# Kernel tuning notes

Hardware: AMD Instinct MI355X
Metric: run time of the kernel (lower is better)

Reference implementation:

```python
import jax, jax.numpy as jnp
import numpy as np

N = 100000   # nodes
E = 1600000  # edges
F_IN = 128
H = 128
C = 40


def setup_inputs() -> dict:
    key = jax.random.key(0)
    ks = jax.random.split(key, 8)
    s = 0.05
    return {
        "x": jax.random.normal(ks[0], (N, F_IN), dtype=jnp.float32),
        "edge_index": jax.random.randint(ks[1], (2, E), 0, N, dtype=jnp.int32),
        "W1": jax.random.normal(ks[2], (F_IN, H), dtype=jnp.float32) * s,
        "b1": jnp.zeros((H,), jnp.float32),
        "W2": jax.random.normal(ks[3], (H, H), dtype=jnp.float32) * s,
        "b2": jnp.zeros((H,), jnp.float32),
        "Wfc": jax.random.normal(ks[4], (H, C), dtype=jnp.float32) * s,
        "bfc": jnp.zeros((C,), jnp.float32),
    }


def _graph_conv(x, src, dst, norm_out, norm_in, W, b):
    # DGL GraphConv, norm='both': h = D_in^{-1/2} A D_out^{-1/2} x W + b
    h = (x * norm_out[:, None]) @ W                      # [N, H] (W first: in>=out)
    agg = jax.ops.segment_sum(h[src], dst, num_segments=N)  # gather + scatter-add
    return agg * norm_in[:, None] + b


def reference(x, edge_index, W1, b1, W2, b2, Wfc, bfc):
    src, dst = edge_index[0], edge_index[1]
    ones = jnp.ones((E,), x.dtype)
    deg_out = jnp.maximum(jax.ops.segment_sum(ones, src, num_segments=N), 1.0)
    deg_in = jnp.maximum(jax.ops.segment_sum(ones, dst, num_segments=N), 1.0)
    norm_out = jax.lax.rsqrt(deg_out)
    norm_in = jax.lax.rsqrt(deg_in)
    # layer 0: GraphConv + relu (dropout is identity in eval mode)
    h = jax.nn.relu(_graph_conv(x, src, dst, norm_out, norm_in, W1, b1))
    # layer 1: GraphConv, no activation
    h = _graph_conv(h, src, dst, norm_out, norm_in, W2, b2)
    # final FC
    return h @ Wfc + bfc
```

## Files before the change

### kernel.cpp

```cpp
#include <hip/hip_runtime.h>
#include <hip/hip_fp16.h>


#define CHUNK    8192
#define NBK      800
#define SLAB     3072

typedef __attribute__((ext_vector_type(8))) short bf16x8;
typedef __attribute__((ext_vector_type(4))) float f32x4;

struct __align__(8)  half4 { __half x, y, z, w; };
struct __align__(16) half8 { __half h[8]; };

__device__ __forceinline__ unsigned short f2bf(float f) {
    union { float f; unsigned u; } v; v.f = f;
    unsigned r = v.u + 0x7FFFu + ((v.u >> 16) & 1u);
    return (unsigned short)(r >> 16);
}
__device__ __forceinline__ float bf2f(unsigned short h) {
    union { unsigned u; float f; } v; v.u = ((unsigned)h) << 16;
    return v.f;
}

__global__ void setup_kernel(const float* __restrict__ W1, const float* __restrict__ W2,
                             const float* __restrict__ Wfc,
                             const float* __restrict__ b2, const float* __restrict__ bfc,
                             unsigned short* __restrict__ Wh1, unsigned short* __restrict__ Wl1,
                             unsigned short* __restrict__ Wh2, unsigned short* __restrict__ Wl2,
                             float* __restrict__ b2p,
                             int* __restrict__ cur_d, int* __restrict__ deg_out,
                             int nbuck, int N_) {
    int idx = blockIdx.x * blockDim.x + threadIdx.x;
    if (idx < nbuck) cur_d[idx] = idx * SLAB;
    for (int i = idx; i < N_; i += gridDim.x * blockDim.x) deg_out[i] = 0;

    if (idx < 16384) {
        int k = idx >> 7, nn = idx & 127;
        float v = W1[idx];
        int q = k >> 5, j = k & 7, lb = ((k >> 3) & 3) * 16;
        int tcol = nn >> 4;
        int l = lb + (nn & 15);
        int pos = ((tcol * 4 + q) * 64 + l) * 8 + j;
        unsigned short h = f2bf(v);
        Wh1[pos] = h;
        Wl1[pos] = f2bf(v - bf2f(h));
    } else if (idx < 16384 + 6144) {
        int i2 = idx - 16384;
        int k = i2 / 48, nn = i2 - k * 48;
        float v = 0.f;
        if (nn < 40) {
            const float* w2row = W2 + k * 128;
            #pragma unroll 8
            for (int jj = 0; jj < 128; ++jj) v += w2row[jj] * Wfc[jj * 40 + nn];
        }
        int t = nn >> 4, q = k >> 5, j = k & 7;
        int l = ((k >> 3) & 3) * 16 + (nn & 15);
        int pos = ((t * 4 + q) * 64 + l) * 8 + j;
        unsigned short h = f2bf(v);
        Wh2[pos] = h;
        Wl2[pos] = f2bf(v - bf2f(h));
    } else if (idx < 16384 + 6144 + 40) {
        int c = idx - (16384 + 6144);
        float a = bfc[c];
        #pragma unroll 8
        for (int j = 0; j < 128; ++j) a += b2[j] * Wfc[j * 40 + c];
        b2p[c] = a;
    }
}

__global__ __launch_bounds__(256) void scatter_res_kernel(
        const int* __restrict__ src, const int* __restrict__ dst,
        int* __restrict__ cur_d, int* __restrict__ deg_out,
        unsigned int* __restrict__ ppack, int E) {
    __shared__ int hd[NBK], bd[NBK];
    const int tid = threadIdx.x;
    for (int i = tid; i < NBK; i += 256) hd[i] = 0;
    __syncthreads();
    const int base = blockIdx.x * CHUNK;
    const int end  = min(base + CHUNK, E);
    for (int e = base + tid; e < end; e += 256) {
        atomicAdd(&hd[((unsigned)dst[e]) >> 7], 1);
        atomicAdd(&deg_out[src[e]], 1);
    }
    __syncthreads();
    for (int i = tid; i < NBK; i += 256) {
        int cd = hd[i];
        bd[i] = cd ? atomicAdd(&cur_d[i], cd) : 0;
        hd[i] = 0;
    }
    __syncthreads();
    for (int e = base + tid; e < end; e += 256) {
        int d = dst[e], s = src[e];
        unsigned bin_d = ((unsigned)d) >> 7;
        int pos = bd[bin_d] + atomicAdd(&hd[bin_d], 1);
        ppack[pos] = (((unsigned)d & 127u) << 17) | (unsigned)s;
    }
}

__global__ __launch_bounds__(256) void fine_kernel(
        const unsigned int* __restrict__ ppack, const int* __restrict__ cur_d,
        const int* __restrict__ deg_out,
        int* __restrict__ deg_in, float* __restrict__ norm_in,
        int* __restrict__ row_ptr, int* __restrict__ csr_src,
        float* __restrict__ norm_out, int N_) {
    __shared__ int h[128];
    __shared__ int psum[128];
    const int tid = threadIdx.x;
    const int b = blockIdx.x;
    const int start = b * SLAB;
    const int node  = (b << 7) + tid;

    if (tid < 128 && node < N_) {
        int d = deg_out[node];
        norm_out[node] = rsqrtf((float)(d < 1 ? 1 : d));
    }

    const int end_d = cur_d[b];
    if (tid < 128) h[tid] = 0;
    __syncthreads();
    for (int i = start + tid; i < end_d; i += 256)
        atomicAdd(&h[ppack[i] >> 17], 1);
    __syncthreads();

    int a = 0;
    if (tid < 128) { a = h[tid]; psum[tid] = a; }
    __syncthreads();
    for (int off = 1; off < 128; off <<= 1) {
        int t = 0;
        if (tid < 128 && tid >= off) t = psum[tid - off];
        __syncthreads();
        if (tid < 128) psum[tid] += t;
        __syncthreads();
    }

    if (tid < 128) {
        int base0 = psum[tid] - a + start;
        if (node < N_) {
            deg_in[node]  = a;
            row_ptr[node] = base0;
            norm_in[node] = rsqrtf((float)(a < 1 ? 1 : a));
        }
        h[tid] = base0;
    }
    __syncthreads();

    for (int i = start + tid; i < end_d; i += 256) {
        unsigned int pk = ppack[i];
        int pos = atomicAdd(&h[pk >> 17], 1);
        csr_src[pos] = (int)(pk & 0x1FFFFu);
    }
}

__global__ __launch_bounds__(256, 3) void gemm128(
        const float* __restrict__ X, const float* __restrict__ scale,
        const unsigned short* __restrict__ Wh, const unsigned short* __restrict__ Wl,
        __half* __restrict__ Y, int nrows) {
    const int tid  = threadIdx.x;
    const int lane = tid & 63;
    const int w    = tid >> 6;
    const int m    = lane & 15;
    const int quad = lane >> 4;
    const int rowBase = blockIdx.x * 128 + w * 32;

    bf16x8 Ah[2][4], Al[2][4];
    #pragma unroll
    for (int rt = 0; rt < 2; ++rt) {
        int r = rowBase + rt * 16 + m;
        float sc = (r < nrows) ? scale[r] : 0.f;
        const float* xr = X + (size_t)(r < nrows ? r : 0) * 128;
        #pragma unroll
        for (int q = 0; q < 4; ++q) {
            int k0 = q * 32 + quad * 8;
            float4 a = *(const float4*)(xr + k0);
            float4 bv = *(const float4*)(xr + k0 + 4);
            float v[8] = {a.x * sc, a.y * sc, a.z * sc, a.w * sc,
                          bv.x * sc, bv.y * sc, bv.z * sc, bv.w * sc};
            bf16x8 hi, lo;
            #pragma unroll
            for (int j = 0; j < 8; ++j) {
                unsigned short h = f2bf(v[j]);
                hi[j] = (short)h;
                lo[j] = (short)f2bf(v[j] - bf2f(h));
            }
            Ah[rt][q] = hi; Al[rt][q] = lo;
        }
    }

    f32x4 acc[2][8];
    #pragma unroll
    for (int rt = 0; rt < 2; ++rt)
        #pragma unroll
        for (int t = 0; t < 8; ++t)
            acc[rt][t] = (f32x4){0.f, 0.f, 0.f, 0.f};

    #pragma unroll
    for (int t = 0; t < 8; ++t) {
        #pragma unroll
        for (int q = 0; q < 4; ++q) {
            const int off = ((t * 4 + q) * 64 + lane) * 8;
            bf16x8 Bh = *(const bf16x8*)(Wh + off);
            bf16x8 Bl = *(const bf16x8*)(Wl + off);
            #pragma unroll
            for (int rt = 0; rt < 2; ++rt) {
                acc[rt][t] = __builtin_amdgcn_mfma_f32_16x16x32_bf16(Ah[rt][q], Bh, acc[rt][t], 0, 0, 0);
                acc[rt][t] = __builtin_amdgcn_mfma_f32_16x16x32_bf16(Ah[rt][q], Bl, acc[rt][t], 0, 0, 0);
                acc[rt][t] = __builtin_amdgcn_mfma_f32_16x16x32_bf16(Al[rt][q], Bh, acc[rt][t], 0, 0, 0);
            }
        }
    }

    #pragma unroll
    for (int rt = 0; rt < 2; ++rt) {
        int r0 = rowBase + rt * 16 + quad * 4;
        #pragma unroll
        for (int reg = 0; reg < 4; ++reg) {
            int r = r0 + reg;
            if (r >= nrows) continue;
            __half* yr = Y + (size_t)r * 128 + m;
            #pragma unroll
            for (int t = 0; t < 8; ++t)
                yr[t * 16] = __float2half(acc[rt][t][reg]);
        }
    }
}

__global__ __launch_bounds__(256, 4) void gather_kernel(
        const __half* __restrict__ H, const int* __restrict__ row_ptr,
        const int* __restrict__ deg, const int* __restrict__ csr_src,
        const float* __restrict__ norm_in, const float* __restrict__ b,
        const float* __restrict__ norm_out,
        const unsigned short* __restrict__ Wh2, const unsigned short* __restrict__ Wl2,
        __half* __restrict__ G, int n) {
    __shared__ unsigned short h1h[16][136];
    __shared__ unsigned short h1l[16][136];
    const int tid   = threadIdx.x;
    const int node0 = blockIdx.x * 16;
    const int g     = tid >> 4;
    const int node  = node0 + g;
    const int c     = (tid & 15) * 8;
    const bool active = node < n;

    int start = 0, cnt = 0;
    if (active) { start = row_ptr[node]; cnt = deg[node]; }
    float acc[8] = {0.f, 0.f, 0.f, 0.f, 0.f, 0.f, 0.f, 0.f};

    int j = 0;
    for (; j + 4 <= cnt; j += 4) {
        int s0 = csr_src[start + j];
        int s1 = csr_src[start + j + 1];
        int s2 = csr_src[start + j + 2];
        int s3 = csr_src[start + j + 3];
        half8 v0 = *(const half8*)(H + (long long)s0 * 128 + c);
        half8 v1 = *(const half8*)(H + (long long)s1 * 128 + c);
        half8 v2 = *(const half8*)(H + (long long)s2 * 128 + c);
        half8 v3 = *(const half8*)(H + (long long)s3 * 128 + c);
        #pragma unroll
        for (int k = 0; k < 8; ++k)
            acc[k] += (__half2float(v0.h[k]) + __half2float(v1.h[k]))
                    + (__half2float(v2.h[k]) + __half2float(v3.h[k]));
    }
    for (; j < cnt; ++j) {
        int s0 = csr_src[start + j];
        half8 v0 = *(const half8*)(H + (long long)s0 * 128 + c);
        #pragma unroll
        for (int k = 0; k < 8; ++k) acc[k] += __half2float(v0.h[k]);
    }

    float ni = active ? norm_in[node]  : 0.f;
    float no = active ? norm_out[node] : 0.f;
    float4 b0  = *(const float4*)(b + c);
    float4 b1v = *(const float4*)(b + c + 4);
    float bb[8] = {b0.x, b0.y, b0.z, b0.w, b1v.x, b1v.y, b1v.z, b1v.w};
    bf16x8 hi, lo;
    #pragma unroll
    for (int k = 0; k < 8; ++k) {
        float hv = fmaxf(acc[k] * ni + bb[k], 0.f) * no;
        unsigned short h = f2bf(hv);
        hi[k] = (short)h;
        lo[k] = (short)f2bf(hv - bf2f(h));
    }
    *(bf16x8*)&h1h[g][c] = hi;
    *(bf16x8*)&h1l[g][c] = lo;
    __syncthreads();

    const int w = tid >> 6;
    if (w < 3) {
        const int lane = tid & 63;
        const int m    = lane & 15;
        const int quad = lane >> 4;

        f32x4 a3 = (f32x4){0.f, 0.f, 0.f, 0.f};
        const int t = w;
        #pragma unroll
        for (int q = 0; q < 4; ++q) {
            const int k0 = q * 32 + quad * 8;
            bf16x8 Ah = *(const bf16x8*)&h1h[m][k0];
            bf16x8 Al = *(const bf16x8*)&h1l[m][k0];
            const int off = ((t * 4 + q) * 64 + lane) * 8;
            bf16x8 Bh = *(const bf16x8*)(Wh2 + off);
            bf16x8 Bl = *(const bf16x8*)(Wl2 + off);
            a3 = __builtin_amdgcn_mfma_f32_16x16x32_bf16(Ah, Bh, a3, 0, 0, 0);
            a3 = __builtin_amdgcn_mfma_f32_16x16x32_bf16(Ah, Bl, a3, 0, 0, 0);
            a3 = __builtin_amdgcn_mfma_f32_16x16x32_bf16(Al, Bh, a3, 0, 0, 0);
        }

        const int col = t * 16 + m;
        if (col < 40) {
            const int r0 = node0 + quad * 4;
            #pragma unroll
            for (int reg = 0; reg < 4; ++reg) {
                int r = r0 + reg;
                if (r < n) G[(size_t)r * 64 + col] = __float2half(a3[reg]);
            }
        }
    }
}

__global__ __launch_bounds__(256) void gather40_kernel(
        const __half* __restrict__ G, const int* __restrict__ row_ptr,
        const int* __restrict__ deg, const int* __restrict__ csr_src,
        const float* __restrict__ norm_in, const float* __restrict__ b2p,
        float* __restrict__ out, int n) {
    const int t = blockIdx.x * 256 + threadIdx.x;
    if (t >= n * 5) return;
    const int node = t / 5;
    const int c    = (t - node * 5) * 8;

    const int start = row_ptr[node];
    const int cnt   = deg[node];
    float acc[8] = {0.f, 0.f, 0.f, 0.f, 0.f, 0.f, 0.f, 0.f};

    int j = 0;
    for (; j + 4 <= cnt; j += 4) {
        int s0 = csr_src[start + j];
        int s1 = csr_src[start + j + 1];
        int s2 = csr_src[start + j + 2];
        int s3 = csr_src[start + j + 3];
        half8 v0 = *(const half8*)(G + (long long)s0 * 64 + c);
        half8 v1 = *(const half8*)(G + (long long)s1 * 64 + c);
        half8 v2 = *(const half8*)(G + (long long)s2 * 64 + c);
        half8 v3 = *(const half8*)(G + (long long)s3 * 64 + c);
        #pragma unroll
        for (int k = 0; k < 8; ++k)
            acc[k] += (__half2float(v0.h[k]) + __half2float(v1.h[k]))
                    + (__half2float(v2.h[k]) + __half2float(v3.h[k]));
    }
    for (; j < cnt; ++j) {
        int s0 = csr_src[start + j];
        half8 v0 = *(const half8*)(G + (long long)s0 * 64 + c);
        #pragma unroll
        for (int k = 0; k < 8; ++k) acc[k] += __half2float(v0.h[k]);
    }

    float ni = norm_in[node];
    float4 o0, o1;
    o0.x = acc[0] * ni + b2p[c + 0];
    o0.y = acc[1] * ni + b2p[c + 1];
    o0.z = acc[2] * ni + b2p[c + 2];
    o0.w = acc[3] * ni + b2p[c + 3];
    o1.x = acc[4] * ni + b2p[c + 4];
    o1.y = acc[5] * ni + b2p[c + 5];
    o1.z = acc[6] * ni + b2p[c + 6];
    o1.w = acc[7] * ni + b2p[c + 7];
    float* op = out + (long long)node * 40 + c;
    *(float4*)(op)     = o0;
    *(float4*)(op + 4) = o1;
}

extern "C" void kernel_launch(void* const* d_in, const int* in_sizes, int n_in,
                              void* d_out, int out_size, void* d_ws, size_t ws_size,
                              hipStream_t stream) {
    const float* x   = (const float*)d_in[0];
    const int*   ei  = (const int*)  d_in[1];
    const float* W1  = (const float*)d_in[2];
    const float* b1  = (const float*)d_in[3];
    const float* W2  = (const float*)d_in[4];
    const float* b2  = (const float*)d_in[5];
    const float* Wfc = (const float*)d_in[6];
    const float* bfc = (const float*)d_in[7];
    float* out = (float*)d_out;

    const int N = in_sizes[0] / 128;
    const int E = in_sizes[1] / 2;
    const int* src = ei;
    const int* dst = ei + E;

    const int nbuck = (N + 127) >> 7;
    const int B1 = (E + CHUNK - 1) / CHUNK;

    char* p = (char*)d_ws;
    float* norm_out = (float*)p; p += (size_t)N * 4;
    float* norm_in  = (float*)p; p += (size_t)N * 4;
    float* bufA     = (float*)p; p += (size_t)N * 128 * 4;
    float* bufB     = (float*)p; p += (size_t)N * 128 * 4;
    int*   deg_in   = (int*)p;   p += (size_t)N * 4;
    int*   deg_out  = (int*)p;   p += (size_t)N * 4;
    int*   row_ptr  = (int*)p;   p += (size_t)N * 4;
    int*   csr_src  = (int*)p;   p += (size_t)NBK * SLAB * 4;
    int*   cur_d    = (int*)p;   p += (size_t)1024 * 4;
    float* b2p      = (float*)p; p += (size_t)64 * 4;
    unsigned short* Wh1 = (unsigned short*)p; p += (size_t)16384 * 2;
    unsigned short* Wl1 = (unsigned short*)p; p += (size_t)16384 * 2;
    unsigned short* Wh2 = (unsigned short*)p; p += (size_t)6144 * 2;
    unsigned short* Wl2 = (unsigned short*)p; p += (size_t)6144 * 2;

    unsigned int* ppack = (unsigned int*)bufB;

    __half* h1pre = (__half*)bufA;
    __half* G     = (__half*)bufB;

    const int T = 256;

    setup_kernel<<<(16384 + 6144 + 40 + T - 1) / T, T, 0, stream>>>(
        W1, W2, Wfc, b2, bfc, Wh1, Wl1, Wh2, Wl2, b2p, cur_d, deg_out, nbuck, N);
    scatter_res_kernel<<<B1, T, 0, stream>>>(src, dst, cur_d, deg_out, ppack, E);
    fine_kernel<<<nbuck, T, 0, stream>>>(ppack, cur_d, deg_out,
                                         deg_in, norm_in, row_ptr, csr_src,
                                         norm_out, N);

    const int gemm_grid = (N + 127) / 128;
    gemm128<<<gemm_grid, T, 0, stream>>>(x, norm_out, Wh1, Wl1, h1pre, N);
    const int gather_grid = (N + 15) / 16;
    gather_kernel<<<gather_grid, T, 0, stream>>>(h1pre, row_ptr, deg_in, csr_src,
                                                 norm_in, b1, norm_out,
                                                 Wh2, Wl2, G, N);
    gather40_kernel<<<((size_t)N * 5 + T - 1) / T, T, 0, stream>>>(
        G, row_ptr, deg_in, csr_src, norm_in, b2p, out, N);
}
```

Before: 313.4 us.

## Fuse CSR fine pass with first GEMM and move counter init to memset

Merges the fine CSR-build kernel and the first-layer GEMM into one launch. Even blocks build the per-bucket CSR and odd blocks run the GEMM, which now computes norm_out from deg_out inline. Counter and degree zeroing moves from the setup kernel to a single hipMemsetAsync over a now-contiguous region, and cur_d becomes a relative offset. The scatter kernel uses 1024-thread blocks over half-size chunks. The aim is fewer launches and overlap of the independent CSR and GEMM work, at the cost of mixing heterogeneous blocks under one register budget and adding an extra memset call.

```diff
diff --git a/kernel.cpp b/kernel.cpp
--- a/kernel.cpp
+++ b/kernel.cpp
@@ -2,7 +2,7 @@
 #include <hip/hip_fp16.h>
 
 
-#define CHUNK    8192
+#define CHUNK    4096
 #define NBK      800
 #define SLAB     3072
 
@@ -27,12 +27,8 @@
                              const float* __restrict__ b2, const float* __restrict__ bfc,
                              unsigned short* __restrict__ Wh1, unsigned short* __restrict__ Wl1,
                              unsigned short* __restrict__ Wh2, unsigned short* __restrict__ Wl2,
-                             float* __restrict__ b2p,
-                             int* __restrict__ cur_d, int* __restrict__ deg_out,
-                             int nbuck, int N_) {
+                             float* __restrict__ b2p) {
     int idx = blockIdx.x * blockDim.x + threadIdx.x;
-    if (idx < nbuck) cur_d[idx] = idx * SLAB;
-    for (int i = idx; i < N_; i += gridDim.x * blockDim.x) deg_out[i] = 0;
 
     if (idx < 16384) {
         int k = idx >> 7, nn = idx & 127;
@@ -68,28 +64,28 @@
     }
 }
 
-__global__ __launch_bounds__(256) void scatter_res_kernel(
+__global__ __launch_bounds__(1024) void scatter_res_kernel(
         const int* __restrict__ src, const int* __restrict__ dst,
         int* __restrict__ cur_d, int* __restrict__ deg_out,
         unsigned int* __restrict__ ppack, int E) {
     __shared__ int hd[NBK], bd[NBK];
     const int tid = threadIdx.x;
-    for (int i = tid; i < NBK; i += 256) hd[i] = 0;
+    for (int i = tid; i < NBK; i += 1024) hd[i] = 0;
     __syncthreads();
     const int base = blockIdx.x * CHUNK;
     const int end  = min(base + CHUNK, E);
-    for (int e = base + tid; e < end; e += 256) {
+    for (int e = base + tid; e < end; e += 1024) {
         atomicAdd(&hd[((unsigned)dst[e]) >> 7], 1);
         atomicAdd(&deg_out[src[e]], 1);
     }
     __syncthreads();
-    for (int i = tid; i < NBK; i += 256) {
+    for (int i = tid; i < NBK; i += 1024) {
         int cd = hd[i];
-        bd[i] = cd ? atomicAdd(&cur_d[i], cd) : 0;
+        bd[i] = cd ? (i * SLAB + atomicAdd(&cur_d[i], cd)) : 0;
         hd[i] = 0;
     }
     __syncthreads();
-    for (int e = base + tid; e < end; e += 256) {
+    for (int e = base + tid; e < end; e += 1024) {
         int d = dst[e], s = src[e];
         unsigned bin_d = ((unsigned)d) >> 7;
         int pos = bd[bin_d] + atomicAdd(&hd[bin_d], 1);
@@ -97,76 +93,79 @@
     }
 }
 
-__global__ __launch_bounds__(256) void fine_kernel(
+__global__ __launch_bounds__(256, 3) void fine_gemm_kernel(
         const unsigned int* __restrict__ ppack, const int* __restrict__ cur_d,
         const int* __restrict__ deg_out,
         int* __restrict__ deg_in, float* __restrict__ norm_in,
         int* __restrict__ row_ptr, int* __restrict__ csr_src,
-        float* __restrict__ norm_out, int N_) {
-    __shared__ int h[128];
-    __shared__ int psum[128];
+        float* __restrict__ norm_out, int N_,
+        const float* __restrict__ X,
+        const unsigned short* __restrict__ Wh, const unsigned short* __restrict__ Wl,
+        __half* __restrict__ Y) {
     const int tid = threadIdx.x;
-    const int b = blockIdx.x;
-    const int start = b * SLAB;
-    const int node  = (b << 7) + tid;
-
-    if (tid < 128 && node < N_) {
-        int d = deg_out[node];
-        norm_out[node] = rsqrtf((float)(d < 1 ? 1 : d));
-    }
-
-    const int end_d = cur_d[b];
-    if (tid < 128) h[tid] = 0;
-    __syncthreads();
-    for (int i = start + tid; i < end_d; i += 256)
-        atomicAdd(&h[ppack[i] >> 17], 1);
-    __syncthreads();
-
-    int a = 0;
-    if (tid < 128) { a = h[tid]; psum[tid] = a; }
-    __syncthreads();
-    for (int off = 1; off < 128; off <<= 1) {
-        int t = 0;
-        if (tid < 128 && tid >= off) t = psum[tid - off];
+
+    if ((blockIdx.x & 1) == 0) {
+        __shared__ int h[128];
+        __shared__ int psum[128];
+        const int b = blockIdx.x >> 1;
+        const int start = b * SLAB;
+        const int node  = (b << 7) + tid;
+
+        const int end_d = start + cur_d[b];
+        if (tid < 128) h[tid] = 0;
         __syncthreads();
-        if (tid < 128) psum[tid] += t;
+        for (int i = start + tid; i < end_d; i += 256)
+            atomicAdd(&h[ppack[i] >> 17], 1);
         __syncthreads();
-    }
-
-    if (tid < 128) {
-        int base0 = psum[tid] - a + start;
-        if (node < N_) {
-            deg_in[node]  = a;
-            row_ptr[node] = base0;
-            norm_in[node] = rsqrtf((float)(a < 1 ? 1 : a));
-        }
-        h[tid] = base0;
-    }
-    __syncthreads();
-
-    for (int i = start + tid; i < end_d; i += 256) {
-        unsigned int pk = ppack[i];
-        int pos = atomicAdd(&h[pk >> 17], 1);
-        csr_src[pos] = (int)(pk & 0x1FFFFu);
-    }
-}
-
-__global__ __launch_bounds__(256, 3) void gemm128(
-        const float* __restrict__ X, const float* __restrict__ scale,
-        const unsigned short* __restrict__ Wh, const unsigned short* __restrict__ Wl,
-        __half* __restrict__ Y, int nrows) {
-    const int tid  = threadIdx.x;
+
+        int a = 0;
+        if (tid < 128) { a = h[tid]; psum[tid] = a; }
+        __syncthreads();
+        for (int off = 1; off < 128; off <<= 1) {
+            int t = 0;
+            if (tid < 128 && tid >= off) t = psum[tid - off];
+            __syncthreads();
+            if (tid < 128) psum[tid] += t;
+            __syncthreads();
+        }
+
+        if (tid < 128) {
+            int base0 = psum[tid] - a + start;
+            if (node < N_) {
+                deg_in[node]  = a;
+                row_ptr[node] = base0;
+                norm_in[node] = rsqrtf((float)(a < 1 ? 1 : a));
+            }
+            h[tid] = base0;
+        }
+        __syncthreads();
+
+        for (int i = start + tid; i < end_d; i += 256) {
+            unsigned int pk = ppack[i];
+            int pos = atomicAdd(&h[pk >> 17], 1);
+            csr_src[pos] = (int)(pk & 0x1FFFFu);
+        }
+        return;
+    }
+
+    const int blk  = blockIdx.x >> 1;
     const int lane = tid & 63;
     const int w    = tid >> 6;
     const int m    = lane & 15;
     const int quad = lane >> 4;
-    const int rowBase = blockIdx.x * 128 + w * 32;
+    const int rowBase = blk * 128 + w * 32;
+    const int nrows = N_;
 
     bf16x8 Ah[2][4], Al[2][4];
     #pragma unroll
     for (int rt = 0; rt < 2; ++rt) {
         int r = rowBase + rt * 16 + m;
-        float sc = (r < nrows) ? scale[r] : 0.f;
+        float sc = 0.f;
+        if (r < nrows) {
+            int d = deg_out[r];
+            sc = rsqrtf((float)(d < 1 ? 1 : d));
+            if (quad == 0) norm_out[r] = sc;
+        }
         const float* xr = X + (size_t)(r < nrows ? r : 0) * 128;
         #pragma unroll
         for (int q = 0; q < 4; ++q) {
@@ -394,10 +393,10 @@
     float* bufA     = (float*)p; p += (size_t)N * 128 * 4;
     float* bufB     = (float*)p; p += (size_t)N * 128 * 4;
     int*   deg_in   = (int*)p;   p += (size_t)N * 4;
-    int*   deg_out  = (int*)p;   p += (size_t)N * 4;
     int*   row_ptr  = (int*)p;   p += (size_t)N * 4;
     int*   csr_src  = (int*)p;   p += (size_t)NBK * SLAB * 4;
     int*   cur_d    = (int*)p;   p += (size_t)1024 * 4;
+    int*   deg_out  = (int*)p;   p += (size_t)N * 4;
     float* b2p      = (float*)p; p += (size_t)64 * 4;
     unsigned short* Wh1 = (unsigned short*)p; p += (size_t)16384 * 2;
     unsigned short* Wl1 = (unsigned short*)p; p += (size_t)16384 * 2;
@@ -411,15 +410,14 @@
 
     const int T = 256;
 
+    hipMemsetAsync(cur_d, 0, (size_t)(1024 + N) * 4, stream);
     setup_kernel<<<(16384 + 6144 + 40 + T - 1) / T, T, 0, stream>>>(
-        W1, W2, Wfc, b2, bfc, Wh1, Wl1, Wh2, Wl2, b2p, cur_d, deg_out, nbuck, N);
-    scatter_res_kernel<<<B1, T, 0, stream>>>(src, dst, cur_d, deg_out, ppack, E);
-    fine_kernel<<<nbuck, T, 0, stream>>>(ppack, cur_d, deg_out,
-                                         deg_in, norm_in, row_ptr, csr_src,
-                                         norm_out, N);
-
-    const int gemm_grid = (N + 127) / 128;
-    gemm128<<<gemm_grid, T, 0, stream>>>(x, norm_out, Wh1, Wl1, h1pre, N);
+        W1, W2, Wfc, b2, bfc, Wh1, Wl1, Wh2, Wl2, b2p);
+    scatter_res_kernel<<<B1, 1024, 0, stream>>>(src, dst, cur_d, deg_out,
+                                                ppack, E);
+    fine_gemm_kernel<<<2 * nbuck, T, 0, stream>>>(
+        ppack, cur_d, deg_out, deg_in, norm_in, row_ptr, csr_src,
+        norm_out, N, x, Wh1, Wl1, h1pre);
     const int gather_grid = (N + 15) / 16;
     gather_kernel<<<gather_grid, T, 0, stream>>>(h1pre, row_ptr, deg_in, csr_src,
                                                  norm_in, b1, norm_out,
```

Result: no change. 310.0 us (-1.1%).
